# Kernel tuning notes

Hardware: AMD Instinct MI355X
Metric: run time of the kernel (lower is better)

Reference implementation:

```python
import jax, jax.numpy as jnp
import numpy as np

N = 4096   # num_nodes == input_size
F = 4096   # edge feature dim (square here)
OUT = 4096 # output_size


def setup_inputs() -> dict:
    key = jax.random.key(0)
    k1, k2, k3, k4 = jax.random.split(key, 4)
    adjacency_matrix = jax.random.randint(k1, (N, N), 0, 2).astype(jnp.float32)
    edge_features = jax.random.normal(k2, (N, F), dtype=jnp.float32)
    # nn.Linear(input_size=N, output_size=OUT): weight [OUT, N], bias [OUT]
    W = jax.random.normal(k3, (OUT, N), dtype=jnp.float32) / np.sqrt(N)
    b = jax.random.normal(k4, (OUT,), dtype=jnp.float32) / np.sqrt(N)
    return {"adjacency_matrix": adjacency_matrix, "edge_features": edge_features,
            "W": W, "b": b}


def line_graph_adjacency(adjacency_matrix):
    # L[i,j] = 1 iff i != j and exists k with k != i, k != j,
    #          A[i,k] == 1 and A[j,k] == 1.
    M = (adjacency_matrix == 1).astype(jnp.float32)  # [N, N]
    d = jnp.diagonal(M)                              # M[i, i]
    # common-neighbor count over all k, then subtract k == i and k == j terms
    cnt = M @ M.T - d[:, None] * M.T - M * d[None, :]
    n = M.shape[0]
    off_diag = ~jnp.eye(n, dtype=bool)
    return ((cnt > 0) & off_diag).astype(jnp.float32)


def reference(adjacency_matrix, edge_features, W, b):
    L = line_graph_adjacency(adjacency_matrix)       # [N, N]
    messages = L @ edge_features                     # [N, F]
    aggregated = jnp.sum(messages, axis=1)           # [N]
    return aggregated @ W.T + b                      # [OUT]
```

## Files before the change

### kernel.cpp

```cpp
#include <hip/hip_runtime.h>
#include <cstdint>
#include <cstddef>


#define NN     4096
#define NCHUNK 32
#define TI     64
#define STRIPJ 256
#define NTHR   256

typedef unsigned int uint32;
typedef float f32x4 __attribute__((ext_vector_type(4)));

__device__ __forceinline__ float4 ntload4(const float* p) {
  f32x4 v = __builtin_nontemporal_load(reinterpret_cast<const f32x4*>(p));
  return make_float4(v.x, v.y, v.z, v.w);
}

__global__ __launch_bounds__(256) void prep_kernel(const float* __restrict__ A,
                                                   const float* __restrict__ E,
                                                   uint32* __restrict__ bitsT,
                                                   float* __restrict__ e,
                                                   float* __restrict__ agg) {
  const int b = blockIdx.x;
  const int t = threadIdx.x;
  if (b < NN) {
    const int lane = t & 63;
    const int wv   = t >> 6;
    const float* arow = A + (size_t)b * NN;
#pragma unroll
    for (int s0 = 0; s0 < 4; ++s0) {
      const int s = wv + 4 * s0;
      float4 v = ntload4(&arow[s * 256 + 4 * lane]);
      uint32 nib = (v.x == 1.0f ? 1u : 0u) | (v.y == 1.0f ? 2u : 0u)
                 | (v.z == 1.0f ? 4u : 0u) | (v.w == 1.0f ? 8u : 0u);
      uint32 w = nib << (4 * (lane & 7));
      w |= __shfl_xor(w, 1);
      w |= __shfl_xor(w, 2);
      w |= __shfl_xor(w, 4);
      if ((lane & 7) == 0) {
        const int widx = s * 8 + (lane >> 3);
        bitsT[((size_t)(widx >> 2) * NN + b) * 4 + (widx & 3)] = w;
      }
    }
    if (b == 0) {
      float4 z = make_float4(0.f, 0.f, 0.f, 0.f);
      float4* a4 = reinterpret_cast<float4*>(agg);
      for (int k = t; k < NN / 4; k += NTHR) a4[k] = z;
    }
  } else {
    const int r0 = (b - NN) * 2;
    const float* p0 = E + (size_t)r0 * NN;
    const float* p1 = E + (size_t)(r0 + 1) * NN;
    float s0 = 0.f, s1 = 0.f;
#pragma unroll
    for (int it = 0; it < 4; ++it) {
      const int k = (t + it * NTHR) * 4;
      float4 v0 = ntload4(&p0[k]);
      float4 v1 = ntload4(&p1[k]);
      s0 += v0.x + v0.y + v0.z + v0.w;
      s1 += v1.x + v1.y + v1.z + v1.w;
    }
#pragma unroll
    for (int m = 1; m < 64; m <<= 1) { s0 += __shfl_xor(s0, m); s1 += __shfl_xor(s1, m); }
    __shared__ float red0[4], red1[4];
    if ((t & 63) == 0) { red0[t >> 6] = s0; red1[t >> 6] = s1; }
    __syncthreads();
    if (t == 0) {
      e[r0]     = red0[0] + red0[1] + red0[2] + red0[3];
      e[r0 + 1] = red1[0] + red1[1] + red1[2] + red1[3];
    }
  }
}

__global__ __launch_bounds__(256) void cnt_agg_kernel(const uint32* __restrict__ bitsT,
                                                      const float* __restrict__ e,
                                                      float* __restrict__ agg) {
  __shared__ uint4 ic0[TI];
  __shared__ uint4 jc0[STRIPJ];
  __shared__ float es[STRIPJ];

  const int t     = threadIdx.x;
  const int jbase = blockIdx.x * STRIPJ;
  const int i0    = blockIdx.y * TI;
  const uint4* bT4 = reinterpret_cast<const uint4*>(bitsT);

  if (t < TI) ic0[t] = bT4[i0 + t];
  jc0[t] = bT4[jbase + t];
  es[t]  = e[jbase + t];
  __syncthreads();

  const int ty = t >> 4;
  const int tx = t & 15;

  uint4 iw[4];
#pragma unroll
  for (int r = 0; r < 4; ++r) iw[r] = ic0[ty * 4 + r];

  float acc[4] = {0.f, 0.f, 0.f, 0.f};

  for (int jj = 0; jj < STRIPJ / 16; ++jj) {
    const int jl = jj * 16 + tx;
    const int j  = jbase + jl;
    const uint4 jw = jc0[jl];
    const float ej = es[jl];
#pragma unroll
    for (int r = 0; r < 4; ++r) {
      const int i = i0 + ty * 4 + r;
      const int p = __popc(iw[r].x & jw.x) + __popc(iw[r].y & jw.y)
                  + __popc(iw[r].z & jw.z) + __popc(iw[r].w & jw.w);
      if (__builtin_expect(p > 2, 1)) {
        if (i != j) acc[r] += ej;
      } else {
        int cnt = p;
        for (int c = 1; c < NCHUNK; ++c) {
          const uint4 a = bT4[(size_t)c * NN + i];
          const uint4 bb = bT4[(size_t)c * NN + j];
          cnt += __popc(a.x & bb.x) + __popc(a.y & bb.y)
               + __popc(a.z & bb.z) + __popc(a.w & bb.w);
        }
        const uint32 d_i = (bitsT[(((size_t)(i >> 7) * NN) + i) * 4 + ((i >> 5) & 3)] >> (i & 31)) & 1u;
        const uint32 Mji = (bitsT[(((size_t)(i >> 7) * NN) + j) * 4 + ((i >> 5) & 3)] >> (i & 31)) & 1u;
        const uint32 Mij = (bitsT[(((size_t)(j >> 7) * NN) + i) * 4 + ((j >> 5) & 3)] >> (j & 31)) & 1u;
        const uint32 d_j = (bitsT[(((size_t)(j >> 7) * NN) + j) * 4 + ((j >> 5) & 3)] >> (j & 31)) & 1u;
        const int cc = cnt - (int)(d_i * Mji) - (int)(Mij * d_j);
        if (cc > 0 && i != j) acc[r] += ej;
      }
    }
  }

#pragma unroll
  for (int m = 1; m < 16; m <<= 1)
#pragma unroll
    for (int r = 0; r < 4; ++r) acc[r] += __shfl_xor(acc[r], m);
  if (tx == 0) {
#pragma unroll
    for (int r = 0; r < 4; ++r) atomicAdd(&agg[i0 + ty * 4 + r], acc[r]);
  }
}

__global__ __launch_bounds__(256) void matvec_kernel(const float* __restrict__ Wm,
                                                     const float* __restrict__ bvec,
                                                     const float* __restrict__ agg,
                                                     float* __restrict__ out) {
  const int o0 = blockIdx.x * 2;
  const float* w0 = Wm + (size_t)o0 * NN;
  const float* w1 = Wm + (size_t)(o0 + 1) * NN;
  const float4* ap = reinterpret_cast<const float4*>(agg);
  const int t = threadIdx.x;
  float s0 = 0.f, s1 = 0.f;
#pragma unroll
  for (int it = 0; it < 4; ++it) {
    const int k = t + it * NTHR;
    float4 a4 = ap[k];
    float4 x0 = ntload4(&w0[k * 4]);
    float4 x1 = ntload4(&w1[k * 4]);
    s0 += x0.x * a4.x + x0.y * a4.y + x0.z * a4.z + x0.w * a4.w;
    s1 += x1.x * a4.x + x1.y * a4.y + x1.z * a4.z + x1.w * a4.w;
  }
#pragma unroll
  for (int m = 1; m < 64; m <<= 1) { s0 += __shfl_xor(s0, m); s1 += __shfl_xor(s1, m); }
  __shared__ float red0[4], red1[4];
  if ((t & 63) == 0) { red0[t >> 6] = s0; red1[t >> 6] = s1; }
  __syncthreads();
  if (t == 0) {
    out[o0]     = red0[0] + red0[1] + red0[2] + red0[3] + bvec[o0];
    out[o0 + 1] = red1[0] + red1[1] + red1[2] + red1[3] + bvec[o0 + 1];
  }
}

extern "C" void kernel_launch(void* const* d_in, const int* in_sizes, int n_in,
                              void* d_out, int out_size, void* d_ws, size_t ws_size,
                              hipStream_t stream) {
  const float* A  = (const float*)d_in[0];
  const float* E  = (const float*)d_in[1];
  const float* Wm = (const float*)d_in[2];
  const float* bv = (const float*)d_in[3];
  float* out = (float*)d_out;

  uint32* bitsT = (uint32*)d_ws;
  float*  e     = (float*)((char*)d_ws + (2u << 20));
  float*  agg   = (float*)((char*)d_ws + (2u << 20) + 16384);

  prep_kernel<<<NN + NN / 2, NTHR, 0, stream>>>(A, E, bitsT, e, agg);
  cnt_agg_kernel<<<dim3(NN / STRIPJ, NN / TI), NTHR, 0, stream>>>(bitsT, e, agg);
  matvec_kernel<<<NN / 2, NTHR, 0, stream>>>(Wm, bv, agg, out);
}
```

Measured before the change: 192.7 us.

## Fuse line-graph aggregation with W matvec via per-block rank-update atomics

Merges the count/aggregate kernel and the matvec kernel into one launch. Each block computes the aggregated values for 32 rows, then multiplies them by the matching 32-column slice of W for half the outputs and atomically adds the partial dots into an output pre-initialised with the bias. This removes one launch and the agg round trip through global memory. In exchange, the full i-j count work is duplicated across the two output halves, W is read in strided 128-byte column slices, and the number of atomics grows large.

```diff
diff --git a/kernel.cpp b/kernel.cpp
--- a/kernel.cpp
+++ b/kernel.cpp
@@ -5,9 +5,10 @@
 
 #define NN     4096
 #define NCHUNK 32
-#define TI     64
-#define STRIPJ 256
+#define IBLK   32
+#define JHALF  2048
 #define NTHR   256
+#define CTHR   512
 
 typedef unsigned int uint32;
 typedef float f32x4 __attribute__((ext_vector_type(4)));
@@ -19,9 +20,10 @@
 
 __global__ __launch_bounds__(256) void prep_kernel(const float* __restrict__ A,
                                                    const float* __restrict__ E,
+                                                   const float* __restrict__ bvec,
                                                    uint32* __restrict__ bitsT,
                                                    float* __restrict__ e,
-                                                   float* __restrict__ agg) {
+                                                   float* __restrict__ out) {
   const int b = blockIdx.x;
   const int t = threadIdx.x;
   if (b < NN) {
@@ -44,9 +46,7 @@
       }
     }
     if (b == 0) {
-      float4 z = make_float4(0.f, 0.f, 0.f, 0.f);
-      float4* a4 = reinterpret_cast<float4*>(agg);
-      for (int k = t; k < NN / 4; k += NTHR) a4[k] = z;
+      for (int k = t; k < NN; k += NTHR) out[k] = bvec[k];
     }
   } else {
     const int r0 = (b - NN) * 2;
@@ -73,48 +73,49 @@
   }
 }
 
-__global__ __launch_bounds__(256) void cnt_agg_kernel(const uint32* __restrict__ bitsT,
-                                                      const float* __restrict__ e,
-                                                      float* __restrict__ agg) {
-  __shared__ uint4 ic0[TI];
-  __shared__ uint4 jc0[STRIPJ];
-  __shared__ float es[STRIPJ];
+__global__ __launch_bounds__(512) void cnt_rank_kernel(const uint32* __restrict__ bitsT,
+                                                       const float* __restrict__ e,
+                                                       const float* __restrict__ Wm,
+                                                       float* __restrict__ out) {
+  __shared__ uint4 jc0[JHALF];
+  __shared__ float es[JHALF];
+  __shared__ float agg_lds[IBLK];
 
-  const int t     = threadIdx.x;
-  const int jbase = blockIdx.x * STRIPJ;
-  const int i0    = blockIdx.y * TI;
+  const int t  = threadIdx.x;
+  const int os = blockIdx.x;
+  const int ib = blockIdx.y;
+  const int i0 = ib * IBLK;
   const uint4* bT4 = reinterpret_cast<const uint4*>(bitsT);
 
-  if (t < TI) ic0[t] = bT4[i0 + t];
-  jc0[t] = bT4[jbase + t];
-  es[t]  = e[jbase + t];
-  __syncthreads();
+  const int tx = t & 15;
+  const int ty = t >> 4;
+  const int i  = i0 + ty;
+  const uint4 iw = bT4[i];
 
-  const int ty = t >> 4;
-  const int tx = t & 15;
+  float acc = 0.f;
 
-  uint4 iw[4];
-#pragma unroll
-  for (int r = 0; r < 4; ++r) iw[r] = ic0[ty * 4 + r];
+  for (int h = 0; h < NN / JHALF; ++h) {
+    const int jbase = h * JHALF;
+    __syncthreads();
+    for (int k = t; k < JHALF; k += CTHR) {
+      jc0[k] = bT4[jbase + k];
+      es[k]  = e[jbase + k];
+    }
+    __syncthreads();
 
-  float acc[4] = {0.f, 0.f, 0.f, 0.f};
-
-  for (int jj = 0; jj < STRIPJ / 16; ++jj) {
-    const int jl = jj * 16 + tx;
-    const int j  = jbase + jl;
-    const uint4 jw = jc0[jl];
-    const float ej = es[jl];
-#pragma unroll
-    for (int r = 0; r < 4; ++r) {
-      const int i = i0 + ty * 4 + r;
-      const int p = __popc(iw[r].x & jw.x) + __popc(iw[r].y & jw.y)
-                  + __popc(iw[r].z & jw.z) + __popc(iw[r].w & jw.w);
+    for (int jj = 0; jj < JHALF / 16; ++jj) {
+      const int jl = jj * 16 + tx;
+      const int j  = jbase + jl;
+      const uint4 jw = jc0[jl];
+      const float ej = es[jl];
+      const int p = __popc(iw.x & jw.x) + __popc(iw.y & jw.y)
+                  + __popc(iw.z & jw.z) + __popc(iw.w & jw.w);
       if (__builtin_expect(p > 2, 1)) {
-        if (i != j) acc[r] += ej;
+        if (i != j) acc += ej;
       } else {
         int cnt = p;
         for (int c = 1; c < NCHUNK; ++c) {
-          const uint4 a = bT4[(size_t)c * NN + i];
+          const uint4 a  = bT4[(size_t)c * NN + i];
           const uint4 bb = bT4[(size_t)c * NN + j];
           cnt += __popc(a.x & bb.x) + __popc(a.y & bb.y)
                + __popc(a.z & bb.z) + __popc(a.w & bb.w);
@@ -124,48 +125,29 @@
         const uint32 Mij = (bitsT[(((size_t)(j >> 7) * NN) + i) * 4 + ((j >> 5) & 3)] >> (j & 31)) & 1u;
         const uint32 d_j = (bitsT[(((size_t)(j >> 7) * NN) + j) * 4 + ((j >> 5) & 3)] >> (j & 31)) & 1u;
         const int cc = cnt - (int)(d_i * Mji) - (int)(Mij * d_j);
-        if (cc > 0 && i != j) acc[r] += ej;
+        if (cc > 0 && i != j) acc += ej;
       }
     }
   }
 
 #pragma unroll
-  for (int m = 1; m < 16; m <<= 1)
+  for (int m = 1; m < 16; m <<= 1) acc += __shfl_xor(acc, m);
+  if (tx == 0) agg_lds[ty] = acc;
+  __syncthreads();
+
+  const int o0 = os * (NN / 2);
 #pragma unroll
-    for (int r = 0; r < 4; ++r) acc[r] += __shfl_xor(acc[r], m);
-  if (tx == 0) {
+  for (int k = 0; k < (NN / 2) / CTHR; ++k) {
+    const int o = o0 + t + k * CTHR;
+    const float* wrow = Wm + (size_t)o * NN + i0;
+    float dot = 0.f;
 #pragma unroll
-    for (int r = 0; r < 4; ++r) atomicAdd(&agg[i0 + ty * 4 + r], acc[r]);
-  }
-}
-
-__global__ __launch_bounds__(256) void matvec_kernel(const float* __restrict__ Wm,
-                                                     const float* __restrict__ bvec,
-                                                     const float* __restrict__ agg,
-                                                     float* __restrict__ out) {
-  const int o0 = blockIdx.x * 2;
-  const float* w0 = Wm + (size_t)o0 * NN;
-  const float* w1 = Wm + (size_t)(o0 + 1) * NN;
-  const float4* ap = reinterpret_cast<const float4*>(agg);
-  const int t = threadIdx.x;
-  float s0 = 0.f, s1 = 0.f;
-#pragma unroll
-  for (int it = 0; it < 4; ++it) {
-    const int k = t + it * NTHR;
-    float4 a4 = ap[k];
-    float4 x0 = ntload4(&w0[k * 4]);
-    float4 x1 = ntload4(&w1[k * 4]);
-    s0 += x0.x * a4.x + x0.y * a4.y + x0.z * a4.z + x0.w * a4.w;
-    s1 += x1.x * a4.x + x1.y * a4.y + x1.z * a4.z + x1.w * a4.w;
-  }
-#pragma unroll
-  for (int m = 1; m < 64; m <<= 1) { s0 += __shfl_xor(s0, m); s1 += __shfl_xor(s1, m); }
-  __shared__ float red0[4], red1[4];
-  if ((t & 63) == 0) { red0[t >> 6] = s0; red1[t >> 6] = s1; }
-  __syncthreads();
-  if (t == 0) {
-    out[o0]     = red0[0] + red0[1] + red0[2] + red0[3] + bvec[o0];
-    out[o0 + 1] = red1[0] + red1[1] + red1[2] + red1[3] + bvec[o0 + 1];
+    for (int q = 0; q < IBLK / 4; ++q) {
+      float4 w4 = ntload4(&wrow[q * 4]);
+      dot += w4.x * agg_lds[q * 4 + 0] + w4.y * agg_lds[q * 4 + 1]
+           + w4.z * agg_lds[q * 4 + 2] + w4.w * agg_lds[q * 4 + 3];
+    }
+    atomicAdd(&out[o], dot);
   }
 }
 
@@ -180,9 +162,7 @@
 
   uint32* bitsT = (uint32*)d_ws;
   float*  e     = (float*)((char*)d_ws + (2u << 20));
-  float*  agg   = (float*)((char*)d_ws + (2u << 20) + 16384);
 
-  prep_kernel<<<NN + NN / 2, NTHR, 0, stream>>>(A, E, bitsT, e, agg);
-  cnt_agg_kernel<<<dim3(NN / STRIPJ, NN / TI), NTHR, 0, stream>>>(bitsT, e, agg);
-  matvec_kernel<<<NN / 2, NTHR, 0, stream>>>(Wm, bv, agg, out);
+  prep_kernel<<<NN + NN / 2, NTHR, 0, stream>>>(A, E, bv, bitsT, e, out);
+  cnt_rank_kernel<<<dim3(2, NN / IBLK), CTHR, 0, stream>>>(bitsT, e, Wm, out);
 }
```

After: 258.3 us. 1.34x slower.
